# Kernel optimization log

Hardware: AMD Instinct MI355X
Metric: run time of the kernel (lower is better)

The kernel has to match this reference:

```python
import jax, jax.numpy as jnp
import numpy as np

N = 8192          # n_nodes; must equal OUT due to _weight_norm broadcasting
IN = 512          # in_features
OUT = 8192        # out_features
ALPHA = 0.2       # leaky relu negative slope
NEG_INF = -9e15   # mask value used by the torch module


def setup_inputs() -> dict:
    key = jax.random.key(0)
    k1, k2, k3, k4 = jax.random.split(key, 4)
    x = jax.random.normal(k1, (N, IN), jnp.float32)
    adj = jax.random.randint(k2, (N, N), 0, 2, jnp.int32)
    # nn.Linear weight [out_features, in_features]
    W = jax.random.normal(k3, (OUT, IN), jnp.float32) / np.sqrt(IN)
    # attention vector a: [2*out_features, 1], xavier_uniform-ish scale
    a = jax.random.normal(k4, (2 * OUT, 1), jnp.float32) * (1.414 * np.sqrt(2.0 / (2 * OUT + 1)))
    return {"x": x, "adj": adj, "W": W, "a": a}


def reference(x, adj, W, a):
    h = x @ W.T                                   # [N, OUT] (OUT == N)
    # torch._weight_norm(h, g, dim=1) = h * g / ||h||_cols  (norm over dim 0, kept as [1, OUT])
    col_norm = jnp.linalg.norm(h, axis=0, keepdims=True)   # [1, OUT]
    a1 = a[:OUT]                                  # [OUT, 1]
    a2 = a[OUT:]                                  # [OUT, 1]
    wn1 = h * (a1 / col_norm)                     # [N, N]: h[i,j]*a1[i]/norm[j]
    wn2 = h * (a2 / col_norm)                     # [N, N]
    e = jax.nn.leaky_relu(wn1 + wn2.T, ALPHA)     # [N, N]
    scores = jnp.where(adj > 0, e, NEG_INF)
    attention = jax.nn.softmax(scores, axis=1)    # dropout omitted (eval / deterministic)
    return attention @ h                          # [N, OUT]
```

## Files before the change

kernel.cpp:

```cpp
#include <hip/hip_runtime.h>
#include <hip/hip_bf16.h>
#include <stdint.h>

#define NN 8192
#define KIN 512

typedef __attribute__((ext_vector_type(8))) short bfx8;
typedef __attribute__((ext_vector_type(4))) float f32x4;
typedef __attribute__((ext_vector_type(4))) short sh4;

__device__ __forceinline__ float b2f(unsigned short u) {
  union { unsigned int i; float f; } z; z.i = ((unsigned int)u) << 16; return z.f;
}
__device__ __forceinline__ unsigned short f2b(float f) {
  __hip_bfloat16 h = __float2bfloat16(f);
  union { __hip_bfloat16 h; unsigned short u; } z; z.h = h; return z.u;
}

__device__ __forceinline__ void async16(void* lds, const void* g) {
  __builtin_amdgcn_global_load_lds(
      (const __attribute__((address_space(1))) unsigned int*)g,
      (__attribute__((address_space(3))) unsigned int*)lds,
      16, 0, 0);
}

__global__ __launch_bounds__(256)
void cvt_f32_bf16(const float* __restrict__ in, unsigned short* __restrict__ out, int n4) {
  int i = blockIdx.x * 256 + threadIdx.x;
  if (i >= n4) return;
  const float4 v = reinterpret_cast<const float4*>(in)[i];
  sh4 o;
  o.x = (short)f2b(v.x); o.y = (short)f2b(v.y);
  o.z = (short)f2b(v.z); o.w = (short)f2b(v.w);
  reinterpret_cast<sh4*>(out)[i] = o;
}

__global__ __launch_bounds__(256)
void reduce_cvt(const float* __restrict__ P, unsigned short* __restrict__ out, int n4) {
  const int i = blockIdx.x * 256 + threadIdx.x;
  if (i >= n4) return;
  const size_t plane = (size_t)NN * KIN / 4;
  const float4* P4 = reinterpret_cast<const float4*>(P);
  float4 s = P4[i];
#pragma unroll
  for (int sp = 1; sp < 8; ++sp) {
    const float4 v = P4[i + sp * plane];
    s.x += v.x; s.y += v.y; s.z += v.z; s.w += v.w;
  }
  sh4 o;
  o.x = (short)f2b(s.x); o.y = (short)f2b(s.y);
  o.z = (short)f2b(s.z); o.w = (short)f2b(s.w);
  reinterpret_cast<sh4*>(out)[i] = o;
}

__global__ __launch_bounds__(256)
void transpose_cvt(const float* __restrict__ x, unsigned short* __restrict__ xT,
                   int NR, int NC) {
  __shared__ float t[64][65];
  const int i0 = blockIdx.x << 6;
  const int c0 = blockIdx.y << 6;
  const int tid = threadIdx.x;
  const int rl = tid >> 4;
  const int cl = (tid & 15) << 2;
#pragma unroll
  for (int ps = 0; ps < 4; ++ps) {
    const int r = rl + (ps << 4);
    const float4 v = *reinterpret_cast<const float4*>(&x[(size_t)(i0 + r) * NC + c0 + cl]);
    t[r][cl] = v.x; t[r][cl + 1] = v.y; t[r][cl + 2] = v.z; t[r][cl + 3] = v.w;
  }
  __syncthreads();
  const int cr = tid >> 3;
  const int il = (tid & 7) << 3;
#pragma unroll
  for (int ps = 0; ps < 2; ++ps) {
    const int c = cr + (ps << 5);
    bfx8 o;
#pragma unroll
    for (int j = 0; j < 8; ++j) o[j] = (short)f2b(t[il + j][c]);
    *reinterpret_cast<bfx8*>(&xT[(size_t)(c0 + c) * NR + i0 + il]) = o;
  }
}

template<int MODE, int SPLITS>
__global__ __launch_bounds__(256)
void gemm_bt(const unsigned short* __restrict__ A,
             const unsigned short* __restrict__ B,
             void* __restrict__ C,
             const float* __restrict__ rowscale,
             int M, int Nc, int K)
{
  __shared__ unsigned short As[2][128 * 32];
  __shared__ unsigned short Bs[2][128 * 32];

  const int tid  = threadIdx.x;
  const int lane = tid & 63;
  const int wave = tid >> 6;
  const int wr   = wave >> 1, wc = wave & 1;

  const int nwg = gridDim.x;
  const int cpx = nwg >> 3;
  const int bid = blockIdx.x;
  const int swz = (bid & 7) * cpx + (bid >> 3);
  const int bps = nwg / SPLITS;
  const int split = swz / bps;
  const int rem   = swz % bps;
  const int nbn = Nc >> 7;
  const int bm  = (rem / nbn) << 7;
  const int bn  = (rem % nbn) << 7;
  const int klen  = K / SPLITS;
  const int kbase = split * klen;

  const int off0 = (wave << 10) + (lane << 4);
  const int r0   = off0 >> 6;
  const int k0e  = (off0 & 63) >> 1;
  const int r1   = r0 + 64;

  const unsigned short* Ag0 = A + (size_t)(bm + r0) * K + kbase + k0e;
  const unsigned short* Ag1 = A + (size_t)(bm + r1) * K + kbase + k0e;
  const unsigned short* Bg0 = B + (size_t)(bn + r0) * K + kbase + k0e;
  const unsigned short* Bg1 = B + (size_t)(bn + r1) * K + kbase + k0e;

  f32x4 acc[4][4];
#pragma unroll
  for (int m = 0; m < 4; ++m)
#pragma unroll
    for (int n = 0; n < 4; ++n)
      acc[m][n] = (f32x4){0.f, 0.f, 0.f, 0.f};

  const int ldsoff = (wave << 10);

  auto stage = [&](int buf, int kk) {
    char* la = (char*)&As[buf][0] + ldsoff;
    char* lb = (char*)&Bs[buf][0] + ldsoff;
    async16(la,        Ag0 + kk);
    async16(la + 4096, Ag1 + kk);
    async16(lb,        Bg0 + kk);
    async16(lb + 4096, Bg1 + kk);
  };

  stage(0, 0);
  __syncthreads();

  const int nk   = klen >> 5;
  const int arow = (wr << 6) + (lane & 15);
  const int brow = (wc << 6) + (lane & 15);
  const int koff = (lane >> 4) << 3;

  for (int kt = 0; kt < nk; ++kt) {
    const int cur = kt & 1;
    if (kt + 1 < nk) stage(cur ^ 1, (kt + 1) << 5);

    bfx8 af[4], bf[4];
#pragma unroll
    for (int m = 0; m < 4; ++m)
      af[m] = *reinterpret_cast<const bfx8*>(&As[cur][(arow + (m << 4)) * 32 + koff]);
#pragma unroll
    for (int n = 0; n < 4; ++n)
      bf[n] = *reinterpret_cast<const bfx8*>(&Bs[cur][(brow + (n << 4)) * 32 + koff]);

#pragma unroll
    for (int m = 0; m < 4; ++m)
#pragma unroll
      for (int n = 0; n < 4; ++n)
        acc[m][n] = __builtin_amdgcn_mfma_f32_16x16x32_bf16(af[m], bf[n], acc[m][n], 0, 0, 0);

    __syncthreads();
  }

#pragma unroll
  for (int m = 0; m < 4; ++m) {
    const int rowb = bm + (wr << 6) + (m << 4) + ((lane >> 4) << 2);
#pragma unroll
    for (int j = 0; j < 4; ++j) {
      const int r = rowb + j;
      if (MODE == 1) {
        unsigned short* Cb = (unsigned short*)C;
#pragma unroll
        for (int n = 0; n < 4; ++n)
          __builtin_nontemporal_store(f2b(acc[m][n][j]),
              &Cb[(size_t)r * Nc + bn + (wc << 6) + (n << 4) + (lane & 15)]);
      } else if (MODE == 0) {
        const float s = rowscale[r];
        float* Cf = (float*)C;
#pragma unroll
        for (int n = 0; n < 4; ++n)
          __builtin_nontemporal_store(acc[m][n][j] * s,
              &Cf[(size_t)r * Nc + bn + (wc << 6) + (n << 4) + (lane & 15)]);
      } else {
        float* Cf = (float*)C + (size_t)split * M * Nc;
#pragma unroll
        for (int n = 0; n < 4; ++n)
          Cf[(size_t)r * Nc + bn + (wc << 6) + (n << 4) + (lane & 15)] = acc[m][n][j];
      }
    }
  }
}

template<int MODE>
__global__ __launch_bounds__(256)
void row_reduce(const unsigned short* __restrict__ X, float* __restrict__ out, int ncols) {
  const int row = blockIdx.x;
  const unsigned short* xr = X + (size_t)row * ncols;
  float s = 0.f;
  for (int c = threadIdx.x * 8; c < ncols; c += 2048) {
    bfx8 v = *reinterpret_cast<const bfx8*>(xr + c);
#pragma unroll
    for (int j = 0; j < 8; ++j) {
      float f = b2f((unsigned short)v[j]);
      s += (MODE == 0) ? f * f : f;
    }
  }
#pragma unroll
  for (int o = 32; o > 0; o >>= 1) s += __shfl_down(s, o);
  __shared__ float red[4];
  if ((threadIdx.x & 63) == 0) red[threadIdx.x >> 6] = s;
  __syncthreads();
  if (threadIdx.x == 0) {
    float t = red[0] + red[1] + red[2] + red[3];
    out[row] = (MODE == 0) ? (1.0f / sqrtf(t)) : (1.0f / t);
  }
}

__global__ __launch_bounds__(256)
void invert_vec(float* __restrict__ v) {
  const int i = blockIdx.x * 256 + threadIdx.x;
  v[i] = 1.0f / v[i];
}

__global__ __launch_bounds__(256)
void scores_kernel(const unsigned short* __restrict__ hT,
                   const int* __restrict__ adj,
                   const float* __restrict__ a,
                   const float* __restrict__ icn,
                   unsigned short* __restrict__ p,
                   float* __restrict__ rs_raw,
                   int strip)
{
  __shared__ unsigned short T1t[64][72];

  const int tid   = threadIdx.x;
  const int i0    = blockIdx.x << 6;
  const int jbase = blockIdx.y * strip;
  const int ntile = strip >> 6;

  const int slot = tid & 7;
  const int jb   = slot << 3;
  const int il0  = tid >> 3;
  const int i_p0 = i0 + il0;
  const int i_p1 = i_p0 + 32;
  const float a1_0 = a[i_p0], ici_0 = icn[i_p0];
  const float a1_1 = a[i_p1], ici_1 = icn[i_p1];
  float rs0 = 0.f, rs1 = 0.f;

  const int rblk0 = (((jb >> 3) ^ ((il0 >> 3) & 7)) << 3);
  const int rblk1 = (((jb >> 3) ^ (((il0 + 32) >> 3) & 7)) << 3);

  for (int jt = 0; jt < ntile; ++jt) {
    const int j0 = jbase + (jt << 6);
    __syncthreads();
#pragma unroll
    for (int ss = 0; ss < 2; ++ss) {
      const int u  = tid + (ss << 8);
      const int jr = u >> 3;
      const int cb = (u & 7) << 3;
      const bfx8 v = *reinterpret_cast<const bfx8*>(hT + (size_t)(j0 + jr) * NN + i0 + cb);
      const int colp = ((((jr >> 3) ^ (u & 7)) << 3) | (jr & 7));
#pragma unroll
      for (int k = 0; k < 8; ++k) T1t[cb + k][colp] = (unsigned short)v[k];
    }
    __syncthreads();

    const int j = j0 + jb;
    const float4 ic0 = *reinterpret_cast<const float4*>(icn + j);
    const float4 ic1 = *reinterpret_cast<const float4*>(icn + j + 4);
    const float4 a20 = *reinterpret_cast<const float4*>(a + NN + j);
    const float4 a21 = *reinterpret_cast<const float4*>(a + NN + j + 4);
    const float icj[8] = {ic0.x, ic0.y, ic0.z, ic0.w, ic1.x, ic1.y, ic1.z, ic1.w};
    const float a2j[8] = {a20.x, a20.y, a20.z, a20.w, a21.x, a21.y, a21.z, a21.w};

#pragma unroll
    for (int ps = 0; ps < 2; ++ps) {
      const int il   = (ps == 0) ? il0 : il0 + 32;
      const int i    = (ps == 0) ? i_p0 : i_p1;
      const float a1 = (ps == 0) ? a1_0 : a1_1;
      const float ii = (ps == 0) ? ici_0 : ici_1;
      const int rb   = (ps == 0) ? rblk0 : rblk1;

      const bfx8 hijv = *reinterpret_cast<const bfx8*>(&T1t[il][rb]);
      const bfx8 hjiv = *reinterpret_cast<const bfx8*>(hT + (size_t)i * NN + j);
      const int4 ad0  = *reinterpret_cast<const int4*>(adj + (size_t)i * NN + j);
      const int4 ad1  = *reinterpret_cast<const int4*>(adj + (size_t)i * NN + j + 4);
      const int adv[8] = {ad0.x, ad0.y, ad0.z, ad0.w, ad1.x, ad1.y, ad1.z, ad1.w};

      bfx8 o;
      float rs = 0.f;
#pragma unroll
      for (int k = 0; k < 8; ++k) {
        const float hij = b2f((unsigned short)hijv[k]);
        const float hji = b2f((unsigned short)hjiv[k]);
        const float e0  = hij * (a1 * icj[k]) + hji * (a2j[k] * ii);
        const float e   = e0 > 0.f ? e0 : 0.2f * e0;
        const float pv  = (adv[k] > 0) ? __expf(e) : 0.f;
        const unsigned short ub = f2b(pv);
        o[k] = (short)ub;
        rs += b2f(ub);
      }
      *reinterpret_cast<bfx8*>(p + (size_t)i * NN + j) = o;
      if (ps == 0) rs0 += rs; else rs1 += rs;
    }
  }

#pragma unroll
  for (int o = 1; o < 8; o <<= 1) {
    rs0 += __shfl_xor(rs0, o);
    rs1 += __shfl_xor(rs1, o);
  }
  if (slot == 0) {
    atomicAdd(rs_raw + i_p0, rs0);
    atomicAdd(rs_raw + i_p1, rs1);
  }
}

extern "C" void kernel_launch(void* const* d_in, const int* in_sizes, int n_in,
                              void* d_out, int out_size, void* d_ws, size_t ws_size,
                              hipStream_t stream)
{
  (void)in_sizes; (void)n_in; (void)out_size; (void)ws_size;
  const float* x   = (const float*)d_in[0];
  const int*   adj = (const int*)d_in[1];
  const float* W   = (const float*)d_in[2];
  const float* a   = (const float*)d_in[3];
  float* out = (float*)d_out;

  char* ws = (char*)d_ws;
  unsigned short* hT = (unsigned short*)ws;
  unsigned short* p  = (unsigned short*)(ws + 134217728ull);
  unsigned short* xb = p;
  unsigned short* Wb = p + (size_t)NN * KIN;
  unsigned short* Axb = hT;
  unsigned short* xT  = hT + (size_t)NN * KIN;
  unsigned short* Wb2 = hT + 2 * (size_t)NN * KIN;
  float* icn = (float*)(ws + 268435456ull);
  float* irs = (float*)(ws + 268435456ull + 32768ull);
  float* parts = out;

  hipMemsetAsync(irs, 0, NN * sizeof(float), stream);

  const int n4 = NN * KIN / 4;
  cvt_f32_bf16<<<n4 / 256, 256, 0, stream>>>(x, xb, n4);
  cvt_f32_bf16<<<n4 / 256, 256, 0, stream>>>(W, Wb, n4);

  gemm_bt<1, 1><<<4096, 256, 0, stream>>>(Wb, xb, hT, nullptr, NN, NN, KIN);

  row_reduce<0><<<NN, 256, 0, stream>>>(hT, icn, NN);

  scores_kernel<<<dim3(128, 16), 256, 0, stream>>>(hT, adj, a, icn, p, irs, NN / 16);

  invert_vec<<<NN / 256, 256, 0, stream>>>(irs);

  cvt_f32_bf16<<<n4 / 256, 256, 0, stream>>>(W, Wb2, n4);
  transpose_cvt<<<dim3(NN / 64, KIN / 64), 256, 0, stream>>>(x, xT, NN, KIN);

  gemm_bt<2, 8><<<2048, 256, 0, stream>>>(p, xT, parts, nullptr, NN, KIN, NN);

  reduce_cvt<<<n4 / 256, 256, 0, stream>>>(parts, Axb, n4);

  gemm_bt<0, 1><<<4096, 256, 0, stream>>>(Axb, Wb2, out, irs, NN, NN, KIN);
}
```

Measured before the change: 544.0 us.

## Store split-K partials in bf16, fuse x conversions, reuse converted W

The split-K partial outputs of the attention-times-x GEMM are now written and read as bf16 instead of fp32, halving the partial-sum traffic through the reduce kernel. The transpose kernel now also emits the row-major bf16 copy of x, which removes one conversion launch. The bf16 W buffer is kept in a separate workspace region and reused by the final GEMM instead of being reconverted. Rounding each partial to bf16 before summation adds precision loss.

```diff
diff --git a/kernel.cpp b/kernel.cpp
--- a/kernel.cpp
+++ b/kernel.cpp
@@ -36,26 +36,30 @@
 }
 
 __global__ __launch_bounds__(256)
-void reduce_cvt(const float* __restrict__ P, unsigned short* __restrict__ out, int n4) {
+void reduce_cvt(const unsigned short* __restrict__ P, unsigned short* __restrict__ out, int n8) {
   const int i = blockIdx.x * 256 + threadIdx.x;
-  if (i >= n4) return;
-  const size_t plane = (size_t)NN * KIN / 4;
-  const float4* P4 = reinterpret_cast<const float4*>(P);
-  float4 s = P4[i];
+  if (i >= n8) return;
+  const size_t plane = (size_t)NN * KIN / 8;
+  const bfx8* P8 = reinterpret_cast<const bfx8*>(P);
+  bfx8 v = P8[i];
+  float s[8];
+#pragma unroll
+  for (int j = 0; j < 8; ++j) s[j] = b2f((unsigned short)v[j]);
 #pragma unroll
   for (int sp = 1; sp < 8; ++sp) {
-    const float4 v = P4[i + sp * plane];
-    s.x += v.x; s.y += v.y; s.z += v.z; s.w += v.w;
-  }
-  sh4 o;
-  o.x = (short)f2b(s.x); o.y = (short)f2b(s.y);
-  o.z = (short)f2b(s.z); o.w = (short)f2b(s.w);
-  reinterpret_cast<sh4*>(out)[i] = o;
+    const bfx8 w = P8[i + sp * plane];
+#pragma unroll
+    for (int j = 0; j < 8; ++j) s[j] += b2f((unsigned short)w[j]);
+  }
+  bfx8 o;
+#pragma unroll
+  for (int j = 0; j < 8; ++j) o[j] = (short)f2b(s[j]);
+  reinterpret_cast<bfx8*>(out)[i] = o;
 }
 
 __global__ __launch_bounds__(256)
 void transpose_cvt(const float* __restrict__ x, unsigned short* __restrict__ xT,
-                   int NR, int NC) {
+                   unsigned short* __restrict__ xb, int NR, int NC) {
   __shared__ float t[64][65];
   const int i0 = blockIdx.x << 6;
   const int c0 = blockIdx.y << 6;
@@ -67,6 +71,10 @@
     const int r = rl + (ps << 4);
     const float4 v = *reinterpret_cast<const float4*>(&x[(size_t)(i0 + r) * NC + c0 + cl]);
     t[r][cl] = v.x; t[r][cl + 1] = v.y; t[r][cl + 2] = v.z; t[r][cl + 3] = v.w;
+    sh4 o;
+    o.x = (short)f2b(v.x); o.y = (short)f2b(v.y);
+    o.z = (short)f2b(v.z); o.w = (short)f2b(v.w);
+    *reinterpret_cast<sh4*>(&xb[(size_t)(i0 + r) * NC + c0 + cl]) = o;
   }
   __syncthreads();
   const int cr = tid >> 3;
@@ -187,10 +195,10 @@
           __builtin_nontemporal_store(acc[m][n][j] * s,
               &Cf[(size_t)r * Nc + bn + (wc << 6) + (n << 4) + (lane & 15)]);
       } else {
-        float* Cf = (float*)C + (size_t)split * M * Nc;
+        unsigned short* Cb = (unsigned short*)C + (size_t)split * M * Nc;
 #pragma unroll
         for (int n = 0; n < 4; ++n)
-          Cf[(size_t)r * Nc + bn + (wc << 6) + (n << 4) + (lane & 15)] = acc[m][n][j];
+          Cb[(size_t)r * Nc + bn + (wc << 6) + (n << 4) + (lane & 15)] = f2b(acc[m][n][j]);
       }
     }
   }
@@ -335,19 +343,18 @@
   char* ws = (char*)d_ws;
   unsigned short* hT = (unsigned short*)ws;
   unsigned short* p  = (unsigned short*)(ws + 134217728ull);
-  unsigned short* xb = p;
-  unsigned short* Wb = p + (size_t)NN * KIN;
-  unsigned short* Axb = hT;
-  unsigned short* xT  = hT + (size_t)NN * KIN;
-  unsigned short* Wb2 = hT + 2 * (size_t)NN * KIN;
   float* icn = (float*)(ws + 268435456ull);
   float* irs = (float*)(ws + 268435456ull + 32768ull);
-  float* parts = out;
+  unsigned short* xb  = (unsigned short*)(ws + 268435456ull + 65536ull);
+  unsigned short* Wb  = xb + (size_t)NN * KIN;
+  unsigned short* xT  = Wb + (size_t)NN * KIN;
+  unsigned short* Axb = xT + (size_t)NN * KIN;
+  unsigned short* parts = (unsigned short*)out;
 
   hipMemsetAsync(irs, 0, NN * sizeof(float), stream);
 
   const int n4 = NN * KIN / 4;
-  cvt_f32_bf16<<<n4 / 256, 256, 0, stream>>>(x, xb, n4);
+  transpose_cvt<<<dim3(NN / 64, KIN / 64), 256, 0, stream>>>(x, xT, xb, NN, KIN);
   cvt_f32_bf16<<<n4 / 256, 256, 0, stream>>>(W, Wb, n4);
 
   gemm_bt<1, 1><<<4096, 256, 0, stream>>>(Wb, xb, hT, nullptr, NN, NN, KIN);
@@ -358,12 +365,9 @@
 
   invert_vec<<<NN / 256, 256, 0, stream>>>(irs);
 
-  cvt_f32_bf16<<<n4 / 256, 256, 0, stream>>>(W, Wb2, n4);
-  transpose_cvt<<<dim3(NN / 64, KIN / 64), 256, 0, stream>>>(x, xT, NN, KIN);
-
   gemm_bt<2, 8><<<2048, 256, 0, stream>>>(p, xT, parts, nullptr, NN, KIN, NN);
 
-  reduce_cvt<<<n4 / 256, 256, 0, stream>>>(parts, Axb, n4);
-
-  gemm_bt<0, 1><<<4096, 256, 0, stream>>>(Axb, Wb2, out, irs, NN, NN, KIN);
-}
+  reduce_cvt<<<NN * KIN / 8 / 256, 256, 0, stream>>>(parts, Axb, NN * KIN / 8);
+
+  gemm_bt<0, 1><<<4096, 256, 0, stream>>>(Axb, Wb, out, irs, NN, NN, KIN);
+}
```

Measured after the change: 525.3 us. 3.4% less time.
